# Kernel optimization log

Hardware: AMD Instinct MI355X
Metric: run time of the kernel (lower is better)

## Reference

```python
import jax, jax.numpy as jnp
import numpy as np

IN_F = 4096
OUT_F = 4096
SPARSITY = 0.9
NNZ = round((1.0 - SPARSITY) * IN_F * OUT_F)  # 1677722
BATCH = 4096


def setup_inputs() -> dict:
    key = jax.random.key(0)
    k1, k2, k3, k4 = jax.random.split(key, 4)
    x = jax.random.normal(k1, (BATCH, IN_F), dtype=jnp.float32)
    # Kaiming-ish scale for sparse fan-in
    weights = jax.random.normal(k2, (NNZ,), dtype=jnp.float32) * 0.02
    row = jax.random.randint(k3, (NNZ,), 0, OUT_F, dtype=jnp.int32)
    col = jax.random.randint(k4, (NNZ,), 0, IN_F, dtype=jnp.int32)
    indices = jnp.stack([row, col], axis=0)  # (2, nnz) like the torch buffer
    active_mask = jnp.ones((NNZ,), dtype=bool)
    return {
        "x": x,
        "weights": weights,
        "indices": indices,
        "active_mask": active_mask,
        "out_features": OUT_F,
        "in_features": IN_F,
    }


def reference(x, weights, indices, active_mask, out_features, in_features):
    # Torch forward: select active edges, build COO (out,in), coalesce
    # (sums duplicate indices), then y = (W @ x^T)^T.
    # Equivalent math: zero inactive weights, scatter-add into dense W,
    # then a dense matmul. Duplicates are summed by .add, matching coalesce.
    w = jnp.where(active_mask, weights, jnp.zeros((), dtype=weights.dtype))
    W = jnp.zeros((out_features, in_features), dtype=x.dtype)
    W = W.at[indices[0], indices[1]].add(w)  # (out, in)
    return x @ W.T  # (B, out)
```

## Files before the change

kernel.cpp:

```cpp
#include <hip/hip_runtime.h>
#include <cstdint>
#include <cstddef>

#define IN_F  4096
#define OUT_F 4096
#define BATCH 4096

typedef __bf16 bf16_t;
typedef __bf16 bf16x8 __attribute__((ext_vector_type(8)));
typedef float  f32x4  __attribute__((ext_vector_type(4)));

__device__ __forceinline__ unsigned short f32_to_bf16_rne(float f) {
  union { float f; unsigned int u; } v;
  v.f = f;
  unsigned int u = v.u;
  return (unsigned short)((u + 0x7FFFu + ((u >> 16) & 1u)) >> 16);
}

__global__ __launch_bounds__(256) void scatter_kernel(
    const float* __restrict__ w, const int* __restrict__ rows,
    const int* __restrict__ cols, const int* __restrict__ mask,
    float* __restrict__ W, int nnz) {
  int i = blockIdx.x * 256 + threadIdx.x;
  if (i < nnz) {
    if (mask[i] != 0) {
      atomicAdd(&W[(size_t)rows[i] * IN_F + cols[i]], w[i]);
    }
  }
}

__global__ __launch_bounds__(256) void cvt_f32_bf16(
    const float4* __restrict__ in, uint4* __restrict__ out, int n8) {
  int i = blockIdx.x * 256 + threadIdx.x;
  if (i >= n8) return;
  float4 a = in[2 * i];
  float4 b = in[2 * i + 1];
  uint4 o;
  o.x = (unsigned)f32_to_bf16_rne(a.x) | ((unsigned)f32_to_bf16_rne(a.y) << 16);
  o.y = (unsigned)f32_to_bf16_rne(a.z) | ((unsigned)f32_to_bf16_rne(a.w) << 16);
  o.z = (unsigned)f32_to_bf16_rne(b.x) | ((unsigned)f32_to_bf16_rne(b.y) << 16);
  o.w = (unsigned)f32_to_bf16_rne(b.z) | ((unsigned)f32_to_bf16_rne(b.w) << 16);
  out[i] = o;
}

#define A0_B 0
#define B0_B 32768
#define A1_B 65536
#define B1_B 98304
#define HALF 16384

#define STAGE(Xg, kpos, ldsbase) do {                                          \
  __builtin_amdgcn_global_load_lds(                                            \
    (const __attribute__((address_space(1))) void*)((Xg) + (size_t)srow * 4096 + (kpos) + schunk), \
    (__attribute__((address_space(3))) void*)(lds + (ldsbase) + tid * 16), 16, 0, 0); \
  __builtin_amdgcn_global_load_lds(                                            \
    (const __attribute__((address_space(1))) void*)((Xg) + (size_t)(srow + 128) * 4096 + (kpos) + schunk), \
    (__attribute__((address_space(3))) void*)(lds + (ldsbase) + 8192 + tid * 16), 16, 0, 0); \
} while (0)

#define LDA4(base, mh) do {                                                    \
  a0 = *(const bf16x8*)(lds + (base) + offA[mh][0]);                           \
  a1 = *(const bf16x8*)(lds + (base) + offA[mh][1]);                           \
  a2 = *(const bf16x8*)(lds + (base) + offA[mh][2]);                           \
  a3 = *(const bf16x8*)(lds + (base) + offA[mh][3]);                           \
} while (0)

#define LDB4(base) do {                                                        \
  b0 = *(const bf16x8*)(lds + (base) + offB[0]);                               \
  b1 = *(const bf16x8*)(lds + (base) + offB[1]);                               \
  b2 = *(const bf16x8*)(lds + (base) + offB[2]);                               \
  b3 = *(const bf16x8*)(lds + (base) + offB[3]);                               \
} while (0)

#define MFMA16(mh) do {                                                        \
  acc[(mh)*4+0][0] = __builtin_amdgcn_mfma_f32_16x16x32_bf16(a0, b0, acc[(mh)*4+0][0], 0, 0, 0); \
  acc[(mh)*4+0][1] = __builtin_amdgcn_mfma_f32_16x16x32_bf16(a0, b1, acc[(mh)*4+0][1], 0, 0, 0); \
  acc[(mh)*4+0][2] = __builtin_amdgcn_mfma_f32_16x16x32_bf16(a0, b2, acc[(mh)*4+0][2], 0, 0, 0); \
  acc[(mh)*4+0][3] = __builtin_amdgcn_mfma_f32_16x16x32_bf16(a0, b3, acc[(mh)*4+0][3], 0, 0, 0); \
  acc[(mh)*4+1][0] = __builtin_amdgcn_mfma_f32_16x16x32_bf16(a1, b0, acc[(mh)*4+1][0], 0, 0, 0); \
  acc[(mh)*4+1][1] = __builtin_amdgcn_mfma_f32_16x16x32_bf16(a1, b1, acc[(mh)*4+1][1], 0, 0, 0); \
  acc[(mh)*4+1][2] = __builtin_amdgcn_mfma_f32_16x16x32_bf16(a1, b2, acc[(mh)*4+1][2], 0, 0, 0); \
  acc[(mh)*4+1][3] = __builtin_amdgcn_mfma_f32_16x16x32_bf16(a1, b3, acc[(mh)*4+1][3], 0, 0, 0); \
  acc[(mh)*4+2][0] = __builtin_amdgcn_mfma_f32_16x16x32_bf16(a2, b0, acc[(mh)*4+2][0], 0, 0, 0); \
  acc[(mh)*4+2][1] = __builtin_amdgcn_mfma_f32_16x16x32_bf16(a2, b1, acc[(mh)*4+2][1], 0, 0, 0); \
  acc[(mh)*4+2][2] = __builtin_amdgcn_mfma_f32_16x16x32_bf16(a2, b2, acc[(mh)*4+2][2], 0, 0, 0); \
  acc[(mh)*4+2][3] = __builtin_amdgcn_mfma_f32_16x16x32_bf16(a2, b3, acc[(mh)*4+2][3], 0, 0, 0); \
  acc[(mh)*4+3][0] = __builtin_amdgcn_mfma_f32_16x16x32_bf16(a3, b0, acc[(mh)*4+3][0], 0, 0, 0); \
  acc[(mh)*4+3][1] = __builtin_amdgcn_mfma_f32_16x16x32_bf16(a3, b1, acc[(mh)*4+3][1], 0, 0, 0); \
  acc[(mh)*4+3][2] = __builtin_amdgcn_mfma_f32_16x16x32_bf16(a3, b2, acc[(mh)*4+3][2], 0, 0, 0); \
  acc[(mh)*4+3][3] = __builtin_amdgcn_mfma_f32_16x16x32_bf16(a3, b3, acc[(mh)*4+3][3], 0, 0, 0); \
} while (0)

#define BAR()   __builtin_amdgcn_s_barrier()
#define LGKM0() do { asm volatile("s_waitcnt lgkmcnt(0)" ::: "memory");        \
                     __builtin_amdgcn_sched_barrier(0); } while (0)
#define VM(n)   asm volatile("s_waitcnt vmcnt(" #n ")" ::: "memory")
#define PRIO1() __builtin_amdgcn_s_setprio(1)
#define PRIO0() __builtin_amdgcn_s_setprio(0)

__global__ __launch_bounds__(512, 2) void gemm_bt_8ph(
    const bf16_t* __restrict__ A, const bf16_t* __restrict__ Bm,
    float* __restrict__ C) {
  __shared__ __align__(16) char lds[131072];

  const int tid  = threadIdx.x;
  const int lane = tid & 63;
  const int wave = tid >> 6;
  const int wm   = wave >> 2;
  const int wn   = wave & 3;

  const int sbid = (blockIdx.x & 7) * 32 + (blockIdx.x >> 3);
  const int bm   = sbid >> 4;
  const int bn   = sbid & 15;

  const int frow = lane & 15;
  const int c16  = (lane >> 4) * 16;

  int offA[2][4], offB[4];
#pragma unroll
  for (int mh = 0; mh < 2; ++mh)
#pragma unroll
    for (int mi = 0; mi < 4; ++mi) {
      int r = wm * 128 + mh * 64 + mi * 16 + frow;
      offA[mh][mi] = r * 64 + (c16 ^ ((r & 3) << 4));
    }
#pragma unroll
  for (int ni = 0; ni < 4; ++ni) {
    int r = wn * 64 + ni * 16 + frow;
    offB[ni] = r * 64 + (c16 ^ ((r & 3) << 4));
  }

  const int srow   = tid >> 2;
  const int schunk = ((tid & 3) ^ (srow & 3)) * 8;
  const bf16_t* Ag = A  + (size_t)bm * 256 * 4096;
  const bf16_t* Bg = Bm + (size_t)bn * 256 * 4096;

  f32x4 acc[8][4] = {};
  bf16x8 a0, a1, a2, a3, b0, b1, b2, b3;

  STAGE(Ag, 0,  A0_B);
  STAGE(Bg, 0,  B0_B);
  STAGE(Ag, 32, A0_B + HALF);
  STAGE(Bg, 32, B0_B + HALF);
  STAGE(Ag, 64, A1_B);
  STAGE(Bg, 64, B1_B);
  VM(4);
  BAR();

  int kb = 0;
#pragma unroll 1
  for (int i = 0; i < 31; ++i, kb += 128) {
    LDA4(A0_B, 0); LDB4(B0_B);
    STAGE(Ag, kb + 96, A1_B + HALF);
    BAR(); LGKM0(); PRIO1(); MFMA16(0); PRIO0(); BAR();
    LDA4(A0_B, 1);
    STAGE(Bg, kb + 96, B1_B + HALF);
    BAR(); LGKM0(); PRIO1(); MFMA16(1); PRIO0(); BAR();
    LDA4(A0_B + HALF, 0); LDB4(B0_B + HALF);
    STAGE(Ag, kb + 128, A0_B);
    BAR(); LGKM0(); PRIO1(); MFMA16(0); PRIO0(); BAR();
    LDA4(A0_B + HALF, 1);
    STAGE(Bg, kb + 128, B0_B);
    BAR(); LGKM0(); PRIO1(); MFMA16(1); PRIO0(); VM(4); BAR();
    LDA4(A1_B, 0); LDB4(B1_B);
    STAGE(Ag, kb + 160, A0_B + HALF);
    BAR(); LGKM0(); PRIO1(); MFMA16(0); PRIO0(); BAR();
    LDA4(A1_B, 1);
    STAGE(Bg, kb + 160, B0_B + HALF);
    BAR(); LGKM0(); PRIO1(); MFMA16(1); PRIO0(); BAR();
    LDA4(A1_B + HALF, 0); LDB4(B1_B + HALF);
    STAGE(Ag, kb + 192, A1_B);
    BAR(); LGKM0(); PRIO1(); MFMA16(0); PRIO0(); BAR();
    LDA4(A1_B + HALF, 1);
    STAGE(Bg, kb + 192, B1_B);
    BAR(); LGKM0(); PRIO1(); MFMA16(1); PRIO0(); VM(4); BAR();
  }

  LDA4(A0_B, 0); LDB4(B0_B);
  STAGE(Ag, kb + 96, A1_B + HALF);
  BAR(); LGKM0(); PRIO1(); MFMA16(0); PRIO0(); BAR();
  LDA4(A0_B, 1);
  STAGE(Bg, kb + 96, B1_B + HALF);
  BAR(); LGKM0(); PRIO1(); MFMA16(1); PRIO0(); BAR();
  LDA4(A0_B + HALF, 0); LDB4(B0_B + HALF);
  BAR(); LGKM0(); PRIO1(); MFMA16(0); PRIO0(); BAR();
  LDA4(A0_B + HALF, 1);
  BAR(); LGKM0(); PRIO1(); MFMA16(1); PRIO0(); VM(0); BAR();
  LDA4(A1_B, 0); LDB4(B1_B);
  BAR(); LGKM0(); PRIO1(); MFMA16(0); PRIO0(); BAR();
  LDA4(A1_B, 1);
  BAR(); LGKM0(); PRIO1(); MFMA16(1); PRIO0(); BAR();
  LDA4(A1_B + HALF, 0); LDB4(B1_B + HALF);
  BAR(); LGKM0(); PRIO1(); MFMA16(0); PRIO0(); BAR();
  LDA4(A1_B + HALF, 1);
  LGKM0(); PRIO1(); MFMA16(1); PRIO0();

#pragma unroll
  for (int mh = 0; mh < 2; ++mh)
#pragma unroll
    for (int mi = 0; mi < 4; ++mi)
#pragma unroll
      for (int ni = 0; ni < 4; ++ni) {
        const int row = bm * 256 + wm * 128 + mh * 64 + mi * 16 + (lane >> 4) * 4;
        const int col = bn * 256 + wn * 64 + ni * 16 + frow;
#pragma unroll
        for (int jj = 0; jj < 4; ++jj)
          C[(size_t)(row + jj) * 4096 + col] = acc[mh * 4 + mi][ni][jj];
      }
}

extern "C" void kernel_launch(void* const* d_in, const int* in_sizes, int n_in,
                              void* d_out, int out_size, void* d_ws, size_t ws_size,
                              hipStream_t stream) {
  const float* x     = (const float*)d_in[0];
  const float* wvals = (const float*)d_in[1];
  const int*   idx   = (const int*)d_in[2];
  const int*   mk    = (const int*)d_in[3];
  const int    nnz   = in_sizes[1];

  float*  Wf32 = (float*)d_out;
  bf16_t* Wbf  = (bf16_t*)d_ws;
  bf16_t* xbf  = (bf16_t*)((char*)d_ws + (size_t)OUT_F * IN_F * sizeof(bf16_t));

  const size_t needed = (size_t)OUT_F * IN_F * 2 + (size_t)BATCH * IN_F * 2;
  if (ws_size < needed) return;

  hipMemsetAsync(d_out, 0, (size_t)OUT_F * IN_F * sizeof(float), stream);

  scatter_kernel<<<(nnz + 255) / 256, 256, 0, stream>>>(
      wvals, idx, idx + nnz, mk, Wf32, nnz);

  const int w8 = (OUT_F * IN_F) / 8;
  cvt_f32_bf16<<<(w8 + 255) / 256, 256, 0, stream>>>(
      (const float4*)Wf32, (uint4*)Wbf, w8);

  const int x8 = (BATCH * IN_F) / 8;
  cvt_f32_bf16<<<(x8 + 255) / 256, 256, 0, stream>>>(
      (const float4*)x, (uint4*)xbf, x8);

  gemm_bt_8ph<<<256, 512, 0, stream>>>(xbf, Wbf, (float*)d_out);
}
```

Before: 238.3 us.

## Fuse zero-init with x conversion, deepen B prefetch, change LDS swizzle

Replaces the memset and the separate x-to-bf16 conversion launch with one grid-stride kernel that zeroes the fp32 W buffer and converts x, removing a launch. In the GEMM, B tiles are now staged one half-step further ahead, with the vmcnt waits adjusted to match, so global loads overlap more with MFMA work. The LDS XOR swizzle now keys on (row>>1)&3 instead of row&3 to cut bank conflicts. The tail logic is hand-rewritten with fixed offsets and wait counts, so any mismatch in the waits could expose a race.

```diff
diff --git a/kernel.cpp b/kernel.cpp
--- a/kernel.cpp
+++ b/kernel.cpp
@@ -15,6 +15,34 @@
   v.f = f;
   unsigned int u = v.u;
   return (unsigned short)((u + 0x7FFFu + ((u >> 16) & 1u)) >> 16);
+}
+
+__device__ __forceinline__ uint4 cvt8(float4 a, float4 b) {
+  uint4 o;
+  o.x = (unsigned)f32_to_bf16_rne(a.x) | ((unsigned)f32_to_bf16_rne(a.y) << 16);
+  o.y = (unsigned)f32_to_bf16_rne(a.z) | ((unsigned)f32_to_bf16_rne(a.w) << 16);
+  o.z = (unsigned)f32_to_bf16_rne(b.x) | ((unsigned)f32_to_bf16_rne(b.y) << 16);
+  o.w = (unsigned)f32_to_bf16_rne(b.z) | ((unsigned)f32_to_bf16_rne(b.w) << 16);
+  return o;
+}
+
+#define WUNITS ((OUT_F * IN_F) / 8)
+#define XUNITS ((BATCH * IN_F) / 8)
+
+__global__ __launch_bounds__(256) void init_zero_cvtx(
+    float4* __restrict__ Wf32v, const float4* __restrict__ xin,
+    uint4* __restrict__ xbf) {
+  const float4 z = {0.f, 0.f, 0.f, 0.f};
+  for (int u = blockIdx.x * 256 + threadIdx.x; u < WUNITS + XUNITS;
+       u += gridDim.x * 256) {
+    if (u < WUNITS) {
+      Wf32v[2 * u]     = z;
+      Wf32v[2 * u + 1] = z;
+    } else {
+      const int i = u - WUNITS;
+      xbf[i] = cvt8(xin[2 * i], xin[2 * i + 1]);
+    }
+  }
 }
 
 __global__ __launch_bounds__(256) void scatter_kernel(
@@ -33,14 +61,7 @@
     const float4* __restrict__ in, uint4* __restrict__ out, int n8) {
   int i = blockIdx.x * 256 + threadIdx.x;
   if (i >= n8) return;
-  float4 a = in[2 * i];
-  float4 b = in[2 * i + 1];
-  uint4 o;
-  o.x = (unsigned)f32_to_bf16_rne(a.x) | ((unsigned)f32_to_bf16_rne(a.y) << 16);
-  o.y = (unsigned)f32_to_bf16_rne(a.z) | ((unsigned)f32_to_bf16_rne(a.w) << 16);
-  o.z = (unsigned)f32_to_bf16_rne(b.x) | ((unsigned)f32_to_bf16_rne(b.y) << 16);
-  o.w = (unsigned)f32_to_bf16_rne(b.z) | ((unsigned)f32_to_bf16_rne(b.w) << 16);
-  out[i] = o;
+  out[i] = cvt8(in[2 * i], in[2 * i + 1]);
 }
 
 #define A0_B 0
@@ -122,16 +143,16 @@
 #pragma unroll
     for (int mi = 0; mi < 4; ++mi) {
       int r = wm * 128 + mh * 64 + mi * 16 + frow;
-      offA[mh][mi] = r * 64 + (c16 ^ ((r & 3) << 4));
+      offA[mh][mi] = r * 64 + (c16 ^ (((r >> 1) & 3) << 4));
     }
 #pragma unroll
   for (int ni = 0; ni < 4; ++ni) {
     int r = wn * 64 + ni * 16 + frow;
-    offB[ni] = r * 64 + (c16 ^ ((r & 3) << 4));
+    offB[ni] = r * 64 + (c16 ^ (((r >> 1) & 3) << 4));
   }
 
   const int srow   = tid >> 2;
-  const int schunk = ((tid & 3) ^ (srow & 3)) * 8;
+  const int schunk = ((tid & 3) ^ ((srow >> 1) & 3)) * 8;
   const bf16_t* Ag = A  + (size_t)bm * 256 * 4096;
   const bf16_t* Bg = Bm + (size_t)bn * 256 * 4096;
 
@@ -142,9 +163,10 @@
   STAGE(Bg, 0,  B0_B);
   STAGE(Ag, 32, A0_B + HALF);
   STAGE(Bg, 32, B0_B + HALF);
+  STAGE(Bg, 64, B1_B);
   STAGE(Ag, 64, A1_B);
-  STAGE(Bg, 64, B1_B);
-  VM(4);
+  STAGE(Bg, 96, B1_B + HALF);
+  VM(6);
   BAR();
 
   int kb = 0;
@@ -154,42 +176,41 @@
     STAGE(Ag, kb + 96, A1_B + HALF);
     BAR(); LGKM0(); PRIO1(); MFMA16(0); PRIO0(); BAR();
     LDA4(A0_B, 1);
-    STAGE(Bg, kb + 96, B1_B + HALF);
-    BAR(); LGKM0(); PRIO1(); MFMA16(1); PRIO0(); BAR();
+    STAGE(Bg, kb + 128, B0_B);
+    BAR(); LGKM0(); PRIO1(); MFMA16(1); PRIO0(); VM(10); BAR();
     LDA4(A0_B + HALF, 0); LDB4(B0_B + HALF);
     STAGE(Ag, kb + 128, A0_B);
     BAR(); LGKM0(); PRIO1(); MFMA16(0); PRIO0(); BAR();
     LDA4(A0_B + HALF, 1);
-    STAGE(Bg, kb + 128, B0_B);
-    BAR(); LGKM0(); PRIO1(); MFMA16(1); PRIO0(); VM(4); BAR();
+    STAGE(Bg, kb + 160, B0_B + HALF);
+    BAR(); LGKM0(); PRIO1(); MFMA16(1); PRIO0(); VM(10); BAR();
     LDA4(A1_B, 0); LDB4(B1_B);
     STAGE(Ag, kb + 160, A0_B + HALF);
     BAR(); LGKM0(); PRIO1(); MFMA16(0); PRIO0(); BAR();
     LDA4(A1_B, 1);
-    STAGE(Bg, kb + 160, B0_B + HALF);
-    BAR(); LGKM0(); PRIO1(); MFMA16(1); PRIO0(); BAR();
+    STAGE(Bg, kb + 192, B1_B);
+    BAR(); LGKM0(); PRIO1(); MFMA16(1); PRIO0(); VM(10); BAR();
     LDA4(A1_B + HALF, 0); LDB4(B1_B + HALF);
     STAGE(Ag, kb + 192, A1_B);
     BAR(); LGKM0(); PRIO1(); MFMA16(0); PRIO0(); BAR();
     LDA4(A1_B + HALF, 1);
-    STAGE(Bg, kb + 192, B1_B);
-    BAR(); LGKM0(); PRIO1(); MFMA16(1); PRIO0(); VM(4); BAR();
+    STAGE(Bg, kb + 224, B1_B + HALF);
+    BAR(); LGKM0(); PRIO1(); MFMA16(1); PRIO0(); VM(10); BAR();
   }
 
   LDA4(A0_B, 0); LDB4(B0_B);
-  STAGE(Ag, kb + 96, A1_B + HALF);
+  STAGE(Ag, 4064, A1_B + HALF);
   BAR(); LGKM0(); PRIO1(); MFMA16(0); PRIO0(); BAR();
   LDA4(A0_B, 1);
-  STAGE(Bg, kb + 96, B1_B + HALF);
-  BAR(); LGKM0(); PRIO1(); MFMA16(1); PRIO0(); BAR();
+  BAR(); LGKM0(); PRIO1(); MFMA16(1); PRIO0(); VM(6); BAR();
   LDA4(A0_B + HALF, 0); LDB4(B0_B + HALF);
   BAR(); LGKM0(); PRIO1(); MFMA16(0); PRIO0(); BAR();
   LDA4(A0_B + HALF, 1);
+  BAR(); LGKM0(); PRIO1(); MFMA16(1); PRIO0(); VM(2); BAR();
+  LDA4(A1_B, 0); LDB4(B1_B);
+  BAR(); LGKM0(); PRIO1(); MFMA16(0); PRIO0(); BAR();
+  LDA4(A1_B, 1);
   BAR(); LGKM0(); PRIO1(); MFMA16(1); PRIO0(); VM(0); BAR();
-  LDA4(A1_B, 0); LDB4(B1_B);
-  BAR(); LGKM0(); PRIO1(); MFMA16(0); PRIO0(); BAR();
-  LDA4(A1_B, 1);
-  BAR(); LGKM0(); PRIO1(); MFMA16(1); PRIO0(); BAR();
   LDA4(A1_B + HALF, 0); LDB4(B1_B + HALF);
   BAR(); LGKM0(); PRIO1(); MFMA16(0); PRIO0(); BAR();
   LDA4(A1_B + HALF, 1);
@@ -225,7 +246,8 @@
   const size_t needed = (size_t)OUT_F * IN_F * 2 + (size_t)BATCH * IN_F * 2;
   if (ws_size < needed) return;
 
-  hipMemsetAsync(d_out, 0, (size_t)OUT_F * IN_F * sizeof(float), stream);
+  init_zero_cvtx<<<2048, 256, 0, stream>>>(
+      (float4*)Wf32, (const float4*)x, (uint4*)xbf);
 
   scatter_kernel<<<(nnz + 255) / 256, 256, 0, stream>>>(
       wvals, idx, idx + nnz, mk, Wf32, nnz);
@@ -234,9 +256,5 @@
   cvt_f32_bf16<<<(w8 + 255) / 256, 256, 0, stream>>>(
       (const float4*)Wf32, (uint4*)Wbf, w8);
 
-  const int x8 = (BATCH * IN_F) / 8;
-  cvt_f32_bf16<<<(x8 + 255) / 256, 256, 0, stream>>>(
-      (const float4*)x, (uint4*)xbf, x8);
-
   gemm_bt_8ph<<<256, 512, 0, stream>>>(xbf, Wbf, (float*)d_out);
 }
```

New measurement: 227.7 us. 1.05x faster.

## Fuse scatter, conversion and GEMM into one cooperative kernel with bf16 atomics

Applied to the files above, without the earlier changes.

Replaces the memset, fp32 scatter, two conversion kernels and GEMM with a single cooperative kernel that zeroes the bf16 weight buffer, scatters weights directly into bf16 using packed bf16 atomic adds while converting x, then runs the GEMM after grid syncs. This removes the fp32 dense W round trip and several kernel launches. It also changes the LDS swizzle pattern to use (row>>1)&3. Accumulating duplicates in bf16 loses precision versus fp32 accumulation, and grid-wide syncs add overhead.

```diff
diff --git a/kernel.cpp b/kernel.cpp
--- a/kernel.cpp
+++ b/kernel.cpp
@@ -1,6 +1,9 @@
 #include <hip/hip_runtime.h>
+#include <hip/hip_cooperative_groups.h>
 #include <cstdint>
 #include <cstddef>
+
+namespace cg = cooperative_groups;
 
 #define IN_F  4096
 #define OUT_F 4096
@@ -9,6 +12,10 @@
 typedef __bf16 bf16_t;
 typedef __bf16 bf16x8 __attribute__((ext_vector_type(8)));
 typedef float  f32x4  __attribute__((ext_vector_type(4)));
+
+#define WU16   ((OUT_F * IN_F) / 8)
+#define XUNITS ((BATCH * IN_F) / 8)
+#define NTHR   (256 * 512)
 
 __device__ __forceinline__ unsigned short f32_to_bf16_rne(float f) {
   union { float f; unsigned int u; } v;
@@ -17,30 +24,13 @@
   return (unsigned short)((u + 0x7FFFu + ((u >> 16) & 1u)) >> 16);
 }
 
-__global__ __launch_bounds__(256) void scatter_kernel(
-    const float* __restrict__ w, const int* __restrict__ rows,
-    const int* __restrict__ cols, const int* __restrict__ mask,
-    float* __restrict__ W, int nnz) {
-  int i = blockIdx.x * 256 + threadIdx.x;
-  if (i < nnz) {
-    if (mask[i] != 0) {
-      atomicAdd(&W[(size_t)rows[i] * IN_F + cols[i]], w[i]);
-    }
-  }
-}
-
-__global__ __launch_bounds__(256) void cvt_f32_bf16(
-    const float4* __restrict__ in, uint4* __restrict__ out, int n8) {
-  int i = blockIdx.x * 256 + threadIdx.x;
-  if (i >= n8) return;
-  float4 a = in[2 * i];
-  float4 b = in[2 * i + 1];
+__device__ __forceinline__ uint4 cvt8(float4 a, float4 b) {
   uint4 o;
   o.x = (unsigned)f32_to_bf16_rne(a.x) | ((unsigned)f32_to_bf16_rne(a.y) << 16);
   o.y = (unsigned)f32_to_bf16_rne(a.z) | ((unsigned)f32_to_bf16_rne(a.w) << 16);
   o.z = (unsigned)f32_to_bf16_rne(b.x) | ((unsigned)f32_to_bf16_rne(b.y) << 16);
   o.w = (unsigned)f32_to_bf16_rne(b.z) | ((unsigned)f32_to_bf16_rne(b.w) << 16);
-  out[i] = o;
+  return o;
 }
 
 #define A0_B 0
@@ -98,12 +88,52 @@
 #define PRIO1() __builtin_amdgcn_s_setprio(1)
 #define PRIO0() __builtin_amdgcn_s_setprio(0)
 
-__global__ __launch_bounds__(512, 2) void gemm_bt_8ph(
-    const bf16_t* __restrict__ A, const bf16_t* __restrict__ Bm,
+__global__ __launch_bounds__(512, 2) void fused_all(
+    const float4* __restrict__ xin, const float* __restrict__ wvals,
+    const int* __restrict__ idx, const int* __restrict__ mask, int nnz,
+    bf16_t* __restrict__ Wbf, bf16_t* __restrict__ xbf,
     float* __restrict__ C) {
   __shared__ __align__(16) char lds[131072];
 
   const int tid  = threadIdx.x;
+  const int gtid = blockIdx.x * 512 + tid;
+
+  {
+    uint4* Wv = (uint4*)Wbf;
+    const uint4 z = {0u, 0u, 0u, 0u};
+#pragma unroll
+    for (int r = 0; r < WU16 / NTHR; ++r)
+      Wv[gtid + r * NTHR] = z;
+  }
+  cg::this_grid().sync();
+
+  {
+    const int* rows = idx;
+    const int* cols = idx + nnz;
+    uint4* xv = (uint4*)xbf;
+    unsigned* Wpk = (unsigned*)Wbf;
+    const int total = nnz + XUNITS;
+    for (int u = gtid; u < total; u += NTHR) {
+      if (u < nnz) {
+        if (mask[u] != 0) {
+          const unsigned h = f32_to_bf16_rne(wvals[u]);
+          const size_t e = (size_t)rows[u] * IN_F + cols[u];
+          const unsigned data = (e & 1) ? (h << 16) : h;
+          unsigned* p = Wpk + (e >> 1);
+          asm volatile("global_atomic_pk_add_bf16 %0, %1, off"
+                       :: "v"(p), "v"(data) : "memory");
+        }
+      } else {
+        const int i = u - nnz;
+        xv[i] = cvt8(xin[2 * i], xin[2 * i + 1]);
+      }
+    }
+  }
+  cg::this_grid().sync();
+
+  const bf16_t* A  = xbf;
+  const bf16_t* Bm = Wbf;
+
   const int lane = tid & 63;
   const int wave = tid >> 6;
   const int wm   = wave >> 2;
@@ -122,16 +152,16 @@
 #pragma unroll
     for (int mi = 0; mi < 4; ++mi) {
       int r = wm * 128 + mh * 64 + mi * 16 + frow;
-      offA[mh][mi] = r * 64 + (c16 ^ ((r & 3) << 4));
+      offA[mh][mi] = r * 64 + (c16 ^ (((r >> 1) & 3) << 4));
     }
 #pragma unroll
   for (int ni = 0; ni < 4; ++ni) {
     int r = wn * 64 + ni * 16 + frow;
-    offB[ni] = r * 64 + (c16 ^ ((r & 3) << 4));
+    offB[ni] = r * 64 + (c16 ^ (((r >> 1) & 3) << 4));
   }
 
   const int srow   = tid >> 2;
-  const int schunk = ((tid & 3) ^ (srow & 3)) * 8;
+  const int schunk = ((tid & 3) ^ ((srow >> 1) & 3)) * 8;
   const bf16_t* Ag = A  + (size_t)bm * 256 * 4096;
   const bf16_t* Bg = Bm + (size_t)bn * 256 * 4096;
 
@@ -212,31 +242,21 @@
 extern "C" void kernel_launch(void* const* d_in, const int* in_sizes, int n_in,
                               void* d_out, int out_size, void* d_ws, size_t ws_size,
                               hipStream_t stream) {
-  const float* x     = (const float*)d_in[0];
+  const float4* xin  = (const float4*)d_in[0];
   const float* wvals = (const float*)d_in[1];
   const int*   idx   = (const int*)d_in[2];
   const int*   mk    = (const int*)d_in[3];
-  const int    nnz   = in_sizes[1];
-
-  float*  Wf32 = (float*)d_out;
-  bf16_t* Wbf  = (bf16_t*)d_ws;
-  bf16_t* xbf  = (bf16_t*)((char*)d_ws + (size_t)OUT_F * IN_F * sizeof(bf16_t));
+  int          nnz   = in_sizes[1];
+
+  bf16_t* Wbf = (bf16_t*)d_ws;
+  bf16_t* xbf = (bf16_t*)((char*)d_ws + (size_t)OUT_F * IN_F * sizeof(bf16_t));
+  float*  Cout = (float*)d_out;
 
   const size_t needed = (size_t)OUT_F * IN_F * 2 + (size_t)BATCH * IN_F * 2;
   if (ws_size < needed) return;
 
-  hipMemsetAsync(d_out, 0, (size_t)OUT_F * IN_F * sizeof(float), stream);
-
-  scatter_kernel<<<(nnz + 255) / 256, 256, 0, stream>>>(
-      wvals, idx, idx + nnz, mk, Wf32, nnz);
-
-  const int w8 = (OUT_F * IN_F) / 8;
-  cvt_f32_bf16<<<(w8 + 255) / 256, 256, 0, stream>>>(
-      (const float4*)Wf32, (uint4*)Wbf, w8);
-
-  const int x8 = (BATCH * IN_F) / 8;
-  cvt_f32_bf16<<<(x8 + 255) / 256, 256, 0, stream>>>(
-      (const float4*)x, (uint4*)xbf, x8);
-
-  gemm_bt_8ph<<<256, 512, 0, stream>>>(xbf, Wbf, (float*)d_out);
-}
+  void* kargs[] = {(void*)&xin, (void*)&wvals, (void*)&idx, (void*)&mk,
+                   (void*)&nnz, (void*)&Wbf, (void*)&xbf, (void*)&Cout};
+  hipLaunchCooperativeKernel((const void*)fused_all, dim3(256), dim3(512),
+                             kargs, 0, stream);
+}
```

New measurement: 285.5 us. 1.2x slower.

## Scatter directly into bf16 weights with packed atomics and fuse zero/convert passes

Applied to the files above, without the earlier changes.

Replaces the fp32 memset, fp32 atomic scatter and fp32-to-bf16 conversion of W with a single kernel that zeroes the bf16 W buffer and converts x, followed by a scatter that uses packed bf16 atomic adds. This removes a 64MB fp32 intermediate round trip and two launches. It also changes the LDS swizzle pattern in the GEMM to XOR on row pairs. Duplicate indices are now summed in bf16 precision rather than fp32, which adds rounding error.

```diff
diff --git a/kernel.cpp b/kernel.cpp
--- a/kernel.cpp
+++ b/kernel.cpp
@@ -17,30 +17,46 @@
   return (unsigned short)((u + 0x7FFFu + ((u >> 16) & 1u)) >> 16);
 }
 
-__global__ __launch_bounds__(256) void scatter_kernel(
-    const float* __restrict__ w, const int* __restrict__ rows,
-    const int* __restrict__ cols, const int* __restrict__ mask,
-    float* __restrict__ W, int nnz) {
-  int i = blockIdx.x * 256 + threadIdx.x;
-  if (i < nnz) {
-    if (mask[i] != 0) {
-      atomicAdd(&W[(size_t)rows[i] * IN_F + cols[i]], w[i]);
-    }
-  }
-}
-
-__global__ __launch_bounds__(256) void cvt_f32_bf16(
-    const float4* __restrict__ in, uint4* __restrict__ out, int n8) {
-  int i = blockIdx.x * 256 + threadIdx.x;
-  if (i >= n8) return;
-  float4 a = in[2 * i];
-  float4 b = in[2 * i + 1];
+__device__ __forceinline__ uint4 cvt8(float4 a, float4 b) {
   uint4 o;
   o.x = (unsigned)f32_to_bf16_rne(a.x) | ((unsigned)f32_to_bf16_rne(a.y) << 16);
   o.y = (unsigned)f32_to_bf16_rne(a.z) | ((unsigned)f32_to_bf16_rne(a.w) << 16);
   o.z = (unsigned)f32_to_bf16_rne(b.x) | ((unsigned)f32_to_bf16_rne(b.y) << 16);
   o.w = (unsigned)f32_to_bf16_rne(b.z) | ((unsigned)f32_to_bf16_rne(b.w) << 16);
-  out[i] = o;
+  return o;
+}
+
+#define WU16   ((OUT_F * IN_F) / 8)
+#define XUNITS ((BATCH * IN_F) / 8)
+
+__global__ __launch_bounds__(256) void init_zero_cvtx(
+    uint4* __restrict__ Wbfv, const float4* __restrict__ xin,
+    uint4* __restrict__ xbf) {
+  const uint4 z = {0u, 0u, 0u, 0u};
+  for (int u = blockIdx.x * 256 + threadIdx.x; u < WU16 + XUNITS;
+       u += gridDim.x * 256) {
+    if (u < WU16) {
+      Wbfv[u] = z;
+    } else {
+      const int i = u - WU16;
+      xbf[i] = cvt8(xin[2 * i], xin[2 * i + 1]);
+    }
+  }
+}
+
+__global__ __launch_bounds__(256) void scatter_bf16(
+    const float* __restrict__ w, const int* __restrict__ rows,
+    const int* __restrict__ cols, const int* __restrict__ mask,
+    unsigned* __restrict__ Wpk, int nnz) {
+  int i = blockIdx.x * 256 + threadIdx.x;
+  if (i >= nnz) return;
+  if (mask[i] == 0) return;
+  const unsigned h = f32_to_bf16_rne(w[i]);
+  const size_t e = (size_t)rows[i] * IN_F + cols[i];
+  const unsigned data = (e & 1) ? (h << 16) : h;
+  unsigned* p = Wpk + (e >> 1);
+  asm volatile("global_atomic_pk_add_bf16 %0, %1, off"
+               :: "v"(p), "v"(data) : "memory");
 }
 
 #define A0_B 0
@@ -122,16 +138,16 @@
 #pragma unroll
     for (int mi = 0; mi < 4; ++mi) {
       int r = wm * 128 + mh * 64 + mi * 16 + frow;
-      offA[mh][mi] = r * 64 + (c16 ^ ((r & 3) << 4));
+      offA[mh][mi] = r * 64 + (c16 ^ (((r >> 1) & 3) << 4));
     }
 #pragma unroll
   for (int ni = 0; ni < 4; ++ni) {
     int r = wn * 64 + ni * 16 + frow;
-    offB[ni] = r * 64 + (c16 ^ ((r & 3) << 4));
+    offB[ni] = r * 64 + (c16 ^ (((r >> 1) & 3) << 4));
   }
 
   const int srow   = tid >> 2;
-  const int schunk = ((tid & 3) ^ (srow & 3)) * 8;
+  const int schunk = ((tid & 3) ^ ((srow >> 1) & 3)) * 8;
   const bf16_t* Ag = A  + (size_t)bm * 256 * 4096;
   const bf16_t* Bg = Bm + (size_t)bn * 256 * 4096;
 
@@ -218,25 +234,17 @@
   const int*   mk    = (const int*)d_in[3];
   const int    nnz   = in_sizes[1];
 
-  float*  Wf32 = (float*)d_out;
-  bf16_t* Wbf  = (bf16_t*)d_ws;
-  bf16_t* xbf  = (bf16_t*)((char*)d_ws + (size_t)OUT_F * IN_F * sizeof(bf16_t));
+  bf16_t* Wbf = (bf16_t*)d_ws;
+  bf16_t* xbf = (bf16_t*)((char*)d_ws + (size_t)OUT_F * IN_F * sizeof(bf16_t));
 
   const size_t needed = (size_t)OUT_F * IN_F * 2 + (size_t)BATCH * IN_F * 2;
   if (ws_size < needed) return;
 
-  hipMemsetAsync(d_out, 0, (size_t)OUT_F * IN_F * sizeof(float), stream);
-
-  scatter_kernel<<<(nnz + 255) / 256, 256, 0, stream>>>(
-      wvals, idx, idx + nnz, mk, Wf32, nnz);
-
-  const int w8 = (OUT_F * IN_F) / 8;
-  cvt_f32_bf16<<<(w8 + 255) / 256, 256, 0, stream>>>(
-      (const float4*)Wf32, (uint4*)Wbf, w8);
-
-  const int x8 = (BATCH * IN_F) / 8;
-  cvt_f32_bf16<<<(x8 + 255) / 256, 256, 0, stream>>>(
-      (const float4*)x, (uint4*)xbf, x8);
+  init_zero_cvtx<<<2048, 256, 0, stream>>>(
+      (uint4*)Wbf, (const float4*)x, (uint4*)xbf);
+
+  scatter_bf16<<<(nnz + 255) / 256, 256, 0, stream>>>(
+      wvals, idx, idx + nnz, mk, (unsigned*)Wbf, nnz);
 
   gemm_bt_8ph<<<256, 512, 0, stream>>>(xbf, Wbf, (float*)d_out);
 }
```

Result: faster. 209.1 us (-12.3%).
